# Optimization experiments

Measured on AMD Instinct MI355X. Metric: run time of the kernel, lower is better.

## Reference

```python
import jax, jax.numpy as jnp
import numpy as np

B, T, NH, NB = 16, 400, 100, 65
SR, BLOCK = 16000, 160
REV_LEN = SR  # Reverb(sampling_rate, sampling_rate)


def _fft_convolve(signal, kernel):
    # torch: pad signal right by n, kernel left by its length, multiply spectra, keep 2nd half
    n = signal.shape[-1]
    s = jnp.pad(signal, [(0, 0)] * (signal.ndim - 1) + [(0, n)])
    k = jnp.pad(kernel, [(0, 0)] * (kernel.ndim - 1) + [(kernel.shape[-1], 0)])
    out = jnp.fft.irfft(jnp.fft.rfft(s) * jnp.fft.rfft(k), s.shape[-1])
    return out[..., out.shape[-1] // 2:]


def _amp_to_impulse_response(amp, target_size):
    # amp: [..., n_bands] real magnitudes treated as zero-phase rfft coefficients
    ir = jnp.fft.irfft(jax.lax.complex(amp, jnp.zeros_like(amp)))  # [..., 2*(NB-1)]
    fs = ir.shape[-1]
    ir = jnp.roll(ir, fs // 2, axis=-1)
    win = 0.5 - 0.5 * jnp.cos(2.0 * np.pi * jnp.arange(fs, dtype=ir.dtype) / fs)  # periodic hann
    ir = ir * win
    ir = jnp.pad(ir, [(0, 0)] * (ir.ndim - 1) + [(0, target_size - fs)])
    return jnp.roll(ir, -fs // 2, axis=-1)


def setup_inputs() -> dict:
    key = jax.random.key(0)
    ks = jax.random.split(key, 6)
    pitch = 40.0 + 400.0 * jax.random.uniform(ks[0], (B, T, 1), dtype=jnp.float32)
    total_amp = jax.random.uniform(ks[1], (B, T), dtype=jnp.float32)
    harmo_amps = jax.random.uniform(ks[2], (B, NH, T), dtype=jnp.float32) + 1e-3
    noise_filter = 0.1 * jax.random.uniform(ks[3], (B, T, NB), dtype=jnp.float32)
    noise = 2.0 * jax.random.uniform(ks[4], (B, T, BLOCK), dtype=jnp.float32) - 1.0
    reverb_noise = 2.0 * jax.random.uniform(ks[5], (REV_LEN, 1), dtype=jnp.float32) - 1.0
    decay = jnp.asarray(5.0, jnp.float32)
    wet = jnp.asarray(0.0, jnp.float32)
    return dict(pitch=pitch, total_amp=total_amp, harmo_amps=harmo_amps,
                noise_filter=noise_filter, noise=noise, reverb_noise=reverb_noise,
                decay=decay, wet=wet, sampling_rate=SR, block_size=BLOCK)


def reference(pitch, total_amp, harmo_amps, noise_filter, noise, reverb_noise,
              decay, wet, sampling_rate, block_size):
    dt = pitch.dtype
    n_harm = harmo_amps.shape[1]
    harm_idx = jnp.arange(1, n_harm + 1, dtype=dt)
    # remove_above_nyquist: mask harmonics whose freq >= sr/2 (tiny epsilon kept, as in DDSP)
    freqs = pitch[:, :, 0][:, None, :] * harm_idx[None, :, None]          # [B,NH,T]
    aa = (freqs < (sampling_rate / 2)).astype(dt) + 1e-4
    amps = harmo_amps * aa
    amps = jnp.transpose(amps, (0, 2, 1))                                  # [B,T,NH]
    amps = amps / jnp.sum(amps, axis=-1, keepdims=True)
    amps = amps * total_amp[..., None]
    # nearest-neighbor upsample by block_size (F.interpolate default mode)
    amps_up = jnp.repeat(amps, block_size, axis=1)                         # [B,N,NH]
    pitch_up = jnp.repeat(pitch, block_size, axis=1)                       # [B,N,1]
    # harmonic additive synthesis
    omega = jnp.cumsum(2.0 * np.pi * pitch_up / sampling_rate, axis=1)     # [B,N,1]
    harmonic = jnp.sum(jnp.sin(omega * harm_idx) * amps_up, axis=-1, keepdims=True)
    # filtered noise branch
    impulse = _amp_to_impulse_response(noise_filter, block_size)           # [B,T,BLOCK]
    noise_f = _fft_convolve(noise, impulse)                                # [B,T,BLOCK]
    noise_f = noise_f.reshape(noise_f.shape[0], -1, 1)                     # [B,N,1]
    signal = harmonic + noise_f
    # reverb (forward with reverb=True)
    rev_len = reverb_noise.shape[0]
    t = (jnp.arange(rev_len, dtype=dt) / sampling_rate)[None, :, None]     # [1,L,1]
    imp = reverb_noise[None] * jnp.exp(-jax.nn.softplus(-decay) * t * 500.0) * jax.nn.sigmoid(wet)
    imp = imp.at[:, 0].set(1.0)
    imp = jnp.pad(imp, ((0, 0), (0, signal.shape[1] - rev_len), (0, 0)))   # [1,N,1]
    out = _fft_convolve(signal[..., 0], imp[..., 0])[..., None]            # [B,N,1]
    return out
```

## Files before the change

kernel.cpp:

```cpp
#include <hip/hip_runtime.h>

#define B_ 16
#define T_ 400
#define NH_ 100
#define NB_ 65
#define BLK_ 160
#define SR_ 16000
#define N_ 64000
#define REV_ 16000
#define KPAD_ 16128
#define KTOT_ 80128
#define NT_ 1022
#define KSPLIT_ 8
#define STEPS_ 63
#define M_ 8
#define NWG_ 500

typedef __attribute__((ext_vector_type(8))) _Float16 f16x8;
typedef __attribute__((ext_vector_type(2))) _Float16 f16x2;
typedef __attribute__((ext_vector_type(4))) float f32x4;

#define ROT(c, s, c1, s1)                                   \
  {                                                         \
    float _t = (c) * (s1);                                  \
    float _u = (s) * (s1);                                  \
    float _ns = fmaf((s), (c1), _t);                        \
    (c) = fmaf((c), (c1), -_u);                             \
    (s) = _ns;                                              \
  }

static __device__ __forceinline__ float dot2f(f16x2 a, f16x2 b, float c) {
#if __has_builtin(__builtin_amdgcn_fdot2)
  return __builtin_amdgcn_fdot2(a, b, c, false);
#else
  return fmaf((float)a[0], (float)b[0], fmaf((float)a[1], (float)b[1], c));
#endif
}

__global__ __launch_bounds__(512) void k_pre(const float* __restrict__ pitch,
                                             const float* __restrict__ rn,
                                             const float* __restrict__ dec,
                                             const float* __restrict__ wet,
                                             double* __restrict__ Pv,
                                             double* __restrict__ Xv,
                                             _Float16* __restrict__ FH,
                                             _Float16* __restrict__ PH) {
  const int blk = blockIdx.x, tid = threadIdx.x;
  if (blk >= NT_) {
    __shared__ double s[512];
    const int b = blk - NT_, t = tid;
    double x = 0.0;
    if (t < T_) x = (double)pitch[b * T_ + t] * (1.0 / (double)SR_);
    s[t] = x;
    __syncthreads();
    for (int off = 1; off < 512; off <<= 1) {
      double v = (t >= off) ? s[t - off] : 0.0;
      __syncthreads();
      s[t] += v;
      __syncthreads();
    }
    if (t < T_) {
      Xv[b * T_ + t] = x;
      Pv[b * T_ + t] = (s[t] - x) * 160.0;
    }
    return;
  }
  const int t = blk;
  const int gid = t * 512 + tid;
  if (gid < 32256) ((f32x4*)PH)[gid] = (f32x4){0.f, 0.f, 0.f, 0.f};
  const int lane = tid >> 3, j = tid & 7;
  const int idx = (t - 14) * 16 + (lane & 15) - ((lane >> 4) << 3) - j;
  float v = 0.f;
  if (idx == 0) {
    v = 1.0f;
  } else if (idx > 0 && idx < REV_) {
    const float a = log1pf(expf(-dec[0]));
    const float sg = 1.f / (1.f + expf(-wet[0]));
    v = rn[idx] * expf(-a * ((float)idx / (float)SR_) * 500.0f) * sg;
  }
  FH[t * 512 + tid] = (_Float16)v;
}

__global__ __launch_bounds__(160) void k_synth(
    const float* __restrict__ pitch, const float* __restrict__ tamp,
    const float* __restrict__ harmo, const float* __restrict__ nfilt,
    const float* __restrict__ noise, const double* __restrict__ Pv,
    const double* __restrict__ Xv, _Float16* __restrict__ PH) {
  const int bt = blockIdx.x, b = bt / T_, t = bt - b * T_;
  const int tid = threadIdx.x;
  __shared__ __align__(16) float amp[104];
  __shared__ __align__(16) float a_s[NB_ + 3];
  __shared__ __align__(16) float ir_s[68];
  __shared__ __align__(16) _Float16 C0[320];
  __shared__ __align__(16) _Float16 C1[320];
  __shared__ __align__(16) _Float16 imp_sw[128];
  __shared__ float red_s;

  const float pv = pitch[b * T_ + t];
  int nv = (int)(8000.0f / pv);
  if (nv > NH_) nv = NH_;
  while (nv < NH_ && (float)(nv + 1) * pv < 8000.0f) ++nv;
  while (nv > 0 && (float)nv * pv >= 8000.0f) --nv;

  if (tid < NB_) a_s[tid] = nfilt[bt * NB_ + tid];
  {
    const _Float16 nh = (_Float16)noise[bt * BLK_ + tid];
    C0[160 + tid] = nh;
    C1[159 + tid] = nh;
    C0[tid] = (_Float16)0.f;
    if (tid < 159) C1[tid] = (_Float16)0.f;
  }
  if (tid < NH_) {
    const float ha = harmo[(b * NH_ + tid) * T_ + t];
    const float aa = (pv * (float)(tid + 1) < 8000.0f ? 1.0f : 0.0f) + 1e-4f;
    amp[tid] = ha * aa;
  } else if (tid < 104) {
    amp[tid] = 0.f;
  }
  __syncthreads();

  float irv = 0.f;
  if (tid < 65) {
    const float phi = (float)tid * (1.0f / 128.0f);
    const float c1 = __builtin_amdgcn_cosf(phi);
    const float s1 = __builtin_amdgcn_sinf(phi);
    float c2 = fmaf(c1, c1, -s1 * s1), s2 = 2.f * c1 * s1;
    float c3 = fmaf(c2, c1, -s2 * s1), s3 = fmaf(s2, c1, c2 * s1);
    const float c4 = fmaf(c2, c2, -s2 * s2), s4 = 2.f * c2 * s2;
    float r0c = 1.f, r0s = 0.f;
    float r1c = c1, r1s = s1;
    float r2c = c2, r2s = s2;
    float r3c = c3, r3s = s3;
    float a0 = 0.f, a1 = 0.f, a2 = 0.f, a3 = 0.f;
#pragma unroll
    for (int m = 0; m < 16; ++m) {
      const f32x4 a4 = *(const f32x4*)&a_s[m << 2];
      a0 = fmaf(a4[0], r0c, a0); ROT(r0c, r0s, c4, s4);
      a1 = fmaf(a4[1], r1c, a1); ROT(r1c, r1s, c4, s4);
      a2 = fmaf(a4[2], r2c, a2); ROT(r2c, r2s, c4, s4);
      a3 = fmaf(a4[3], r3c, a3); ROT(r3c, r3s, c4, s4);
    }
    const float accS = (a0 + a1) + (a2 + a3);
    irv = (2.f * accS - a_s[0] + ((tid & 1) ? -a_s[64] : a_s[64])) * (1.0f / 128.0f);
    ir_s[tid] = irv;
  } else if (tid >= 128) {
    const int l = tid - 128;
    float v = amp[l] + amp[l + 32] + amp[l + 64] + (l < 4 ? amp[l + 96] : 0.f);
    v += __shfl_xor(v, 16);
    v += __shfl_xor(v, 8);
    v += __shfl_xor(v, 4);
    v += __shfl_xor(v, 2);
    v += __shfl_xor(v, 1);
    if (l == 0) red_s = v;
  }
  __syncthreads();

  if (tid < 64) {
    const float w = 0.5f + 0.5f * __builtin_amdgcn_cosf((float)tid * (1.0f / 128.0f));
    imp_sw[tid ^ 1] = (_Float16)(w * irv);
  } else if (tid >= 96) {
    const int u = tid - 96;
    const float w = 0.5f - 0.5f * __builtin_amdgcn_cosf((float)u * (1.0f / 128.0f));
    imp_sw[64 + (u ^ 1)] = (_Float16)(w * ir_s[64 - u]);
  }
  const float scale = tamp[b * T_ + t] / red_s;
  double th = Pv[bt] + (double)(tid + 1) * Xv[bt];
  th -= floor(th);
  const float theta = (float)th;
  const float cT = __builtin_amdgcn_cosf(theta);
  const float sT = __builtin_amdgcn_sinf(theta);
  __syncthreads();

  float acc;
  {
    float c2 = fmaf(cT, cT, -sT * sT), s2 = 2.f * cT * sT;
    float c3 = fmaf(c2, cT, -s2 * sT), s3 = fmaf(s2, cT, c2 * sT);
    const float c4 = fmaf(c2, c2, -s2 * s2), s4 = 2.f * c2 * s2;
    float rAc = cT, rAs = sT;
    float rBc = c2, rBs = s2;
    float rCc = c3, rCs = s3;
    float rDc = c4, rDs = s4;
    float a0 = 0.f, a1 = 0.f, a2 = 0.f, a3 = 0.f;
    const int S = (nv + 3) >> 2;
    for (int m = 0; m < S; ++m) {
      const f32x4 a4 = *(const f32x4*)&amp[m << 2];
      a0 = fmaf(a4[0], rAs, a0); ROT(rAc, rAs, c4, s4);
      a1 = fmaf(a4[1], rBs, a1); ROT(rBc, rBs, c4, s4);
      a2 = fmaf(a4[2], rCs, a2); ROT(rCc, rCs, c4, s4);
      a3 = fmaf(a4[3], rDs, a3); ROT(rDc, rDs, c4, s4);
    }
    acc = ((a0 + a1) + (a2 + a3)) * scale;
  }

  float nf = 0.f;
  {
    const f16x2* np0;
    int pe;
    if (tid & 1) {
      np0 = (const f16x2*)C0;
      pe = (159 + tid) >> 1;
    } else {
      np0 = (const f16x2*)C1;
      pe = (158 + tid) >> 1;
    }
    const f16x8* ip = (const f16x8*)imp_sw;
#pragma unroll
    for (int k0 = 0; k0 < 8; ++k0) {
      const f16x8 i8 = ip[k0];
      const int kb = k0 << 2;
      nf = dot2f((f16x2){i8[0], i8[1]}, np0[pe - kb], nf);
      nf = dot2f((f16x2){i8[2], i8[3]}, np0[pe - kb - 1], nf);
      nf = dot2f((f16x2){i8[4], i8[5]}, np0[pe - kb - 2], nf);
      nf = dot2f((f16x2){i8[6], i8[7]}, np0[pe - kb - 3], nf);
    }
#pragma unroll
    for (int k0 = 0; k0 < 8; ++k0) {
      const f16x8 i8 = ip[8 + k0];
      const int kb = (k0 << 2) + 48;
      nf = dot2f((f16x2){i8[0], i8[1]}, np0[pe - kb], nf);
      nf = dot2f((f16x2){i8[2], i8[3]}, np0[pe - kb - 1], nf);
      nf = dot2f((f16x2){i8[4], i8[5]}, np0[pe - kb - 2], nf);
      nf = dot2f((f16x2){i8[6], i8[7]}, np0[pe - kb - 3], nf);
    }
  }

  const float v = acc + nf;
  const unsigned k = (unsigned)(KPAD_ + t * BLK_ + tid);
  const unsigned off = ((k >> 3) << 7) + ((unsigned)b << 3) + (k & 7u);
  PH[off] = (_Float16)v;
}

static __device__ __forceinline__ f32x4 mfma_f16(f16x8 a, f16x8 b, f32x4 c) {
  return __builtin_amdgcn_mfma_f32_16x16x32_f16(a, b, c, 0, 0, 0);
}

template <int U, bool PF>
__device__ __forceinline__ void conv_step(f16x8 (&Rh)[M_], f32x4 (&acc)[M_], f16x8& bhi,
                                          const f16x8* __restrict__ ph,
                                          const f16x8* __restrict__ fh,
                                          int& kcur, int& tcur) {
  f16x8 nbh, na0, na1;
  if (PF) {
    kcur += 64;
    nbh = ph[kcur];
    tcur -= 2;
    na0 = fh[tcur * 64];
    na1 = fh[(tcur + 1) * 64];
  }
#pragma unroll
  for (int m = 0; m < M_; ++m) {
    const int sl = (m - 2 * U) & (M_ - 1);
    acc[m] = mfma_f16(Rh[sl], bhi, acc[m]);
  }
  if (PF) {
    Rh[(M_ - 2 - 2 * U) & (M_ - 1)] = na0;
    Rh[(M_ - 1 - 2 * U) & (M_ - 1)] = na1;
    bhi = nbh;
  }
}

__global__ __launch_bounds__(512) void k_mconv(const f16x8* __restrict__ FH,
                                               const f16x8* __restrict__ PH,
                                               float* __restrict__ out) {
  const int tid = threadIdx.x;
  const int s = tid >> 6, lane = tid & 63;
  int w = blockIdx.x;
  {
    const int q = NWG_ / 8, r = NWG_ % 8;
    const int xcd = w & 7, o = w >> 3;
    w = (xcd < r ? xcd * (q + 1) : r * (q + 1) + (xcd - r) * q) + o;
  }
  const int Q0 = w << 7;
  const int T0 = 1014 - 126 * s;

  const f16x8* fh = FH + lane;
  f16x8 Rh[M_];
#pragma unroll
  for (int m = 0; m < M_; ++m) Rh[m] = fh[(T0 + m) * 64];
  f32x4 acc[M_];
#pragma unroll
  for (int m = 0; m < M_; ++m) acc[m] = (f32x4){0.f, 0.f, 0.f, 0.f};

  const f16x8* ph = PH + ((lane >> 4) << 4) + (lane & 15);
  int kcur = (Q0 + 128 + 2016 * s) << 1;
  int tcur = T0;
  f16x8 bhi = ph[kcur];

  for (int ii = 0; ii < 15; ++ii) {
    conv_step<0, true>(Rh, acc, bhi, ph, fh, kcur, tcur);
    conv_step<1, true>(Rh, acc, bhi, ph, fh, kcur, tcur);
    conv_step<2, true>(Rh, acc, bhi, ph, fh, kcur, tcur);
    conv_step<3, true>(Rh, acc, bhi, ph, fh, kcur, tcur);
  }
  conv_step<0, true>(Rh, acc, bhi, ph, fh, kcur, tcur);
  conv_step<1, true>(Rh, acc, bhi, ph, fh, kcur, tcur);
  conv_step<2, false>(Rh, acc, bhi, ph, fh, kcur, tcur);

  __shared__ f32x4 part[4][M_][64];
  if (s < 4) {
#pragma unroll
    for (int m = 0; m < M_; ++m) part[s][m][lane] = acc[m];
  }
  __syncthreads();
  if (s >= 4) {
#pragma unroll
    for (int m = 0; m < M_; ++m) part[s - 4][m][lane] += acc[m];
  }
  __syncthreads();
  {
    const int m = tid >> 6, ln = tid & 63;
    f32x4 v = part[0][m][ln];
    v += part[1][m][ln];
    v += part[2][m][ln];
    v += part[3][m][ln];
    const int b = ln & 15, g = ln >> 4;
    *(f32x4*)(out + (size_t)b * N_ + Q0 + (m << 4) + (g << 2)) = v;
  }
}

extern "C" void kernel_launch(void* const* d_in, const int* in_sizes, int n_in,
                              void* d_out, int out_size, void* d_ws, size_t ws_size,
                              hipStream_t stream) {
  const float* pitch = (const float*)d_in[0];
  const float* tamp  = (const float*)d_in[1];
  const float* harmo = (const float*)d_in[2];
  const float* nfilt = (const float*)d_in[3];
  const float* noise = (const float*)d_in[4];
  const float* rn    = (const float*)d_in[5];
  const float* dec   = (const float*)d_in[6];
  const float* wet   = (const float*)d_in[7];

  char* ws = (char*)d_ws;
  size_t off = 0;
  _Float16* PH = (_Float16*)(ws + off); off += (size_t)KTOT_ * 16 * 2;
  _Float16* FH = (_Float16*)(ws + off); off += (size_t)NT_ * 512 * 2;
  double* Pv = (double*)(ws + off);     off += (size_t)B_ * T_ * 8;
  double* Xv = (double*)(ws + off);     off += (size_t)B_ * T_ * 8;
  float* out = (float*)d_out;

  k_pre<<<dim3(NT_ + B_), dim3(512), 0, stream>>>(pitch, rn, dec, wet, Pv, Xv, FH, PH);
  k_synth<<<dim3(B_ * T_), dim3(160), 0, stream>>>(pitch, tamp, harmo, nfilt, noise, Pv, Xv, PH);
  k_mconv<<<dim3(NWG_), dim3(512), 0, stream>>>((const f16x8*)FH, (const f16x8*)PH, out);
}
```

Before: 71.10 us.

## Use Chebyshev recurrence for harmonic sums and pack two frames per block

Replaces the complex rotation recurrences (four multiplies per step) in the impulse-response DFT and the harmonic sine sum with a Chebyshev three-term recurrence (one FMA per step), handling eight terms per iteration. The synth kernel now processes two frames per 320-thread workgroup, with shared arrays indexed by group, to halve the block count and improve wave packing. The Chebyshev recurrence may accumulate more rounding error than rotation over the roughly 100 harmonics.

```diff
diff --git a/kernel.cpp b/kernel.cpp
--- a/kernel.cpp
+++ b/kernel.cpp
@@ -19,15 +19,6 @@
 typedef __attribute__((ext_vector_type(8))) _Float16 f16x8;
 typedef __attribute__((ext_vector_type(2))) _Float16 f16x2;
 typedef __attribute__((ext_vector_type(4))) float f32x4;
-
-#define ROT(c, s, c1, s1)                                   \
-  {                                                         \
-    float _t = (c) * (s1);                                  \
-    float _u = (s) * (s1);                                  \
-    float _ns = fmaf((s), (c1), _t);                        \
-    (c) = fmaf((c), (c1), -_u);                             \
-    (s) = _ns;                                              \
-  }
 
 static __device__ __forceinline__ float dot2f(f16x2 a, f16x2 b, float c) {
 #if __has_builtin(__builtin_amdgcn_fdot2)
@@ -81,90 +72,98 @@
   FH[t * 512 + tid] = (_Float16)v;
 }
 
-__global__ __launch_bounds__(160) void k_synth(
+__global__ __launch_bounds__(320) void k_synth(
     const float* __restrict__ pitch, const float* __restrict__ tamp,
     const float* __restrict__ harmo, const float* __restrict__ nfilt,
     const float* __restrict__ noise, const double* __restrict__ Pv,
     const double* __restrict__ Xv, _Float16* __restrict__ PH) {
-  const int bt = blockIdx.x, b = bt / T_, t = bt - b * T_;
   const int tid = threadIdx.x;
-  __shared__ __align__(16) float amp[104];
-  __shared__ __align__(16) float a_s[NB_ + 3];
-  __shared__ __align__(16) float ir_s[68];
-  __shared__ __align__(16) _Float16 C0[320];
-  __shared__ __align__(16) _Float16 C1[320];
-  __shared__ __align__(16) _Float16 imp_sw[128];
-  __shared__ float red_s;
-
-  const float pv = pitch[b * T_ + t];
+  const int g = (tid >= 160) ? 1 : 0;
+  const int ltid = tid - (g << 7) - (g << 5);
+  const int bt = (blockIdx.x << 1) + g;
+  const int b = bt / T_, t = bt - b * T_;
+  __shared__ __align__(16) float amp[2][112];
+  __shared__ __align__(16) float a_s[2][68];
+  __shared__ __align__(16) float ir_s[2][68];
+  __shared__ __align__(16) _Float16 C0[2][320];
+  __shared__ __align__(16) _Float16 C1[2][320];
+  __shared__ __align__(16) _Float16 imp_sw[2][128];
+  __shared__ float red_s[2];
+
+  const float pv = pitch[bt];
   int nv = (int)(8000.0f / pv);
   if (nv > NH_) nv = NH_;
   while (nv < NH_ && (float)(nv + 1) * pv < 8000.0f) ++nv;
   while (nv > 0 && (float)nv * pv >= 8000.0f) --nv;
 
-  if (tid < NB_) a_s[tid] = nfilt[bt * NB_ + tid];
-  {
-    const _Float16 nh = (_Float16)noise[bt * BLK_ + tid];
-    C0[160 + tid] = nh;
-    C1[159 + tid] = nh;
-    C0[tid] = (_Float16)0.f;
-    if (tid < 159) C1[tid] = (_Float16)0.f;
-  }
-  if (tid < NH_) {
-    const float ha = harmo[(b * NH_ + tid) * T_ + t];
-    const float aa = (pv * (float)(tid + 1) < 8000.0f ? 1.0f : 0.0f) + 1e-4f;
-    amp[tid] = ha * aa;
-  } else if (tid < 104) {
-    amp[tid] = 0.f;
+  if (ltid < NB_) a_s[g][ltid] = nfilt[bt * NB_ + ltid];
+  {
+    const _Float16 nh = (_Float16)noise[bt * BLK_ + ltid];
+    C0[g][160 + ltid] = nh;
+    C1[g][159 + ltid] = nh;
+    C0[g][ltid] = (_Float16)0.f;
+    if (ltid < 159) C1[g][ltid] = (_Float16)0.f;
+  }
+  if (ltid < NH_) {
+    const float ha = harmo[(b * NH_ + ltid) * T_ + t];
+    const float aa = (pv * (float)(ltid + 1) < 8000.0f ? 1.0f : 0.0f) + 1e-4f;
+    amp[g][ltid] = ha * aa;
+  } else if (ltid < 112) {
+    amp[g][ltid] = 0.f;
   }
   __syncthreads();
 
   float irv = 0.f;
-  if (tid < 65) {
-    const float phi = (float)tid * (1.0f / 128.0f);
+  if (ltid < 65) {
+    const float phi = (float)ltid * (1.0f / 128.0f);
     const float c1 = __builtin_amdgcn_cosf(phi);
-    const float s1 = __builtin_amdgcn_sinf(phi);
-    float c2 = fmaf(c1, c1, -s1 * s1), s2 = 2.f * c1 * s1;
-    float c3 = fmaf(c2, c1, -s2 * s1), s3 = fmaf(s2, c1, c2 * s1);
-    const float c4 = fmaf(c2, c2, -s2 * s2), s4 = 2.f * c2 * s2;
-    float r0c = 1.f, r0s = 0.f;
-    float r1c = c1, r1s = s1;
-    float r2c = c2, r2s = s2;
-    float r3c = c3, r3s = s3;
+    const float c2 = fmaf(2.f * c1, c1, -1.f);
+    const float c3 = fmaf(2.f * c2, c1, -c1);
+    const float c4 = fmaf(2.f * c2, c2, -1.f);
+    const float tc = 2.f * c4;
+    float x0 = 1.f, p0 = c4;
+    float x1 = c1, p1 = c3;
+    float x2 = c2, p2 = c2;
+    float x3 = c3, p3 = c1;
     float a0 = 0.f, a1 = 0.f, a2 = 0.f, a3 = 0.f;
 #pragma unroll
-    for (int m = 0; m < 16; ++m) {
-      const f32x4 a4 = *(const f32x4*)&a_s[m << 2];
-      a0 = fmaf(a4[0], r0c, a0); ROT(r0c, r0s, c4, s4);
-      a1 = fmaf(a4[1], r1c, a1); ROT(r1c, r1s, c4, s4);
-      a2 = fmaf(a4[2], r2c, a2); ROT(r2c, r2s, c4, s4);
-      a3 = fmaf(a4[3], r3c, a3); ROT(r3c, r3s, c4, s4);
+    for (int m = 0; m < 8; ++m) {
+      const f32x4 aA = *(const f32x4*)&a_s[g][m << 3];
+      const f32x4 aB = *(const f32x4*)&a_s[g][(m << 3) + 4];
+      a0 = fmaf(aA[0], x0, a0); const float y0 = fmaf(tc, x0, -p0);
+      a1 = fmaf(aA[1], x1, a1); const float y1 = fmaf(tc, x1, -p1);
+      a2 = fmaf(aA[2], x2, a2); const float y2 = fmaf(tc, x2, -p2);
+      a3 = fmaf(aA[3], x3, a3); const float y3 = fmaf(tc, x3, -p3);
+      a0 = fmaf(aB[0], y0, a0); const float z0 = fmaf(tc, y0, -x0); p0 = y0; x0 = z0;
+      a1 = fmaf(aB[1], y1, a1); const float z1 = fmaf(tc, y1, -x1); p1 = y1; x1 = z1;
+      a2 = fmaf(aB[2], y2, a2); const float z2 = fmaf(tc, y2, -x2); p2 = y2; x2 = z2;
+      a3 = fmaf(aB[3], y3, a3); const float z3 = fmaf(tc, y3, -x3); p3 = y3; x3 = z3;
     }
     const float accS = (a0 + a1) + (a2 + a3);
-    irv = (2.f * accS - a_s[0] + ((tid & 1) ? -a_s[64] : a_s[64])) * (1.0f / 128.0f);
-    ir_s[tid] = irv;
-  } else if (tid >= 128) {
-    const int l = tid - 128;
-    float v = amp[l] + amp[l + 32] + amp[l + 64] + (l < 4 ? amp[l + 96] : 0.f);
+    irv = (2.f * accS - a_s[g][0] + ((ltid & 1) ? -a_s[g][64] : a_s[g][64])) * (1.0f / 128.0f);
+    ir_s[g][ltid] = irv;
+  } else if (ltid >= 128) {
+    const int l = ltid - 128;
+    float v = amp[g][l] + amp[g][l + 32] + amp[g][l + 64] + (l < 4 ? amp[g][l + 96] : 0.f);
     v += __shfl_xor(v, 16);
     v += __shfl_xor(v, 8);
     v += __shfl_xor(v, 4);
     v += __shfl_xor(v, 2);
     v += __shfl_xor(v, 1);
-    if (l == 0) red_s = v;
-  }
-  __syncthreads();
-
-  if (tid < 64) {
-    const float w = 0.5f + 0.5f * __builtin_amdgcn_cosf((float)tid * (1.0f / 128.0f));
-    imp_sw[tid ^ 1] = (_Float16)(w * irv);
-  } else if (tid >= 96) {
-    const int u = tid - 96;
+    if (l == 0) red_s[g] = v;
+  }
+  __syncthreads();
+
+  if (ltid < 64) {
+    const float w = 0.5f + 0.5f * __builtin_amdgcn_cosf((float)ltid * (1.0f / 128.0f));
+    imp_sw[g][ltid ^ 1] = (_Float16)(w * irv);
+  } else if (ltid >= 96 && ltid < 160) {
+    const int u = ltid - 96;
     const float w = 0.5f - 0.5f * __builtin_amdgcn_cosf((float)u * (1.0f / 128.0f));
-    imp_sw[64 + (u ^ 1)] = (_Float16)(w * ir_s[64 - u]);
-  }
-  const float scale = tamp[b * T_ + t] / red_s;
-  double th = Pv[bt] + (double)(tid + 1) * Xv[bt];
+    imp_sw[g][64 + (u ^ 1)] = (_Float16)(w * ir_s[g][64 - u]);
+  }
+  const float scale = tamp[bt] / red_s[g];
+  double th = Pv[bt] + (double)(ltid + 1) * Xv[bt];
   th -= floor(th);
   const float theta = (float)th;
   const float cT = __builtin_amdgcn_cosf(theta);
@@ -173,21 +172,29 @@
 
   float acc;
   {
-    float c2 = fmaf(cT, cT, -sT * sT), s2 = 2.f * cT * sT;
-    float c3 = fmaf(c2, cT, -s2 * sT), s3 = fmaf(s2, cT, c2 * sT);
-    const float c4 = fmaf(c2, c2, -s2 * s2), s4 = 2.f * c2 * s2;
-    float rAc = cT, rAs = sT;
-    float rBc = c2, rBs = s2;
-    float rCc = c3, rCs = s3;
-    float rDc = c4, rDs = s4;
+    const float c2 = fmaf(cT, cT, -sT * sT);
+    const float s2 = 2.f * cT * sT;
+    const float s3 = fmaf(s2, cT, c2 * sT);
+    const float s4 = 2.f * s2 * c2;
+    const float c4 = fmaf(2.f * c2, c2, -1.f);
+    const float tc = 2.f * c4;
+    float x0 = sT, p0 = -s3;
+    float x1 = s2, p1 = -s2;
+    float x2 = s3, p2 = -sT;
+    float x3 = s4, p3 = 0.f;
     float a0 = 0.f, a1 = 0.f, a2 = 0.f, a3 = 0.f;
-    const int S = (nv + 3) >> 2;
+    const int S = (nv + 7) >> 3;
     for (int m = 0; m < S; ++m) {
-      const f32x4 a4 = *(const f32x4*)&amp[m << 2];
-      a0 = fmaf(a4[0], rAs, a0); ROT(rAc, rAs, c4, s4);
-      a1 = fmaf(a4[1], rBs, a1); ROT(rBc, rBs, c4, s4);
-      a2 = fmaf(a4[2], rCs, a2); ROT(rCc, rCs, c4, s4);
-      a3 = fmaf(a4[3], rDs, a3); ROT(rDc, rDs, c4, s4);
+      const f32x4 aA = *(const f32x4*)&amp[g][m << 3];
+      const f32x4 aB = *(const f32x4*)&amp[g][(m << 3) + 4];
+      a0 = fmaf(aA[0], x0, a0); const float y0 = fmaf(tc, x0, -p0);
+      a1 = fmaf(aA[1], x1, a1); const float y1 = fmaf(tc, x1, -p1);
+      a2 = fmaf(aA[2], x2, a2); const float y2 = fmaf(tc, x2, -p2);
+      a3 = fmaf(aA[3], x3, a3); const float y3 = fmaf(tc, x3, -p3);
+      a0 = fmaf(aB[0], y0, a0); const float z0 = fmaf(tc, y0, -x0); p0 = y0; x0 = z0;
+      a1 = fmaf(aB[1], y1, a1); const float z1 = fmaf(tc, y1, -x1); p1 = y1; x1 = z1;
+      a2 = fmaf(aB[2], y2, a2); const float z2 = fmaf(tc, y2, -x2); p2 = y2; x2 = z2;
+      a3 = fmaf(aB[3], y3, a3); const float z3 = fmaf(tc, y3, -x3); p3 = y3; x3 = z3;
     }
     acc = ((a0 + a1) + (a2 + a3)) * scale;
   }
@@ -196,14 +203,14 @@
   {
     const f16x2* np0;
     int pe;
-    if (tid & 1) {
-      np0 = (const f16x2*)C0;
-      pe = (159 + tid) >> 1;
+    if (ltid & 1) {
+      np0 = (const f16x2*)C0[g];
+      pe = (159 + ltid) >> 1;
     } else {
-      np0 = (const f16x2*)C1;
-      pe = (158 + tid) >> 1;
-    }
-    const f16x8* ip = (const f16x8*)imp_sw;
+      np0 = (const f16x2*)C1[g];
+      pe = (158 + ltid) >> 1;
+    }
+    const f16x8* ip = (const f16x8*)imp_sw[g];
 #pragma unroll
     for (int k0 = 0; k0 < 8; ++k0) {
       const f16x8 i8 = ip[k0];
@@ -225,7 +232,7 @@
   }
 
   const float v = acc + nf;
-  const unsigned k = (unsigned)(KPAD_ + t * BLK_ + tid);
+  const unsigned k = (unsigned)(KPAD_ + t * BLK_ + ltid);
   const unsigned off = ((k >> 3) << 7) + ((unsigned)b << 3) + (k & 7u);
   PH[off] = (_Float16)v;
 }
@@ -339,6 +346,6 @@
   float* out = (float*)d_out;
 
   k_pre<<<dim3(NT_ + B_), dim3(512), 0, stream>>>(pitch, rn, dec, wet, Pv, Xv, FH, PH);
-  k_synth<<<dim3(B_ * T_), dim3(160), 0, stream>>>(pitch, tamp, harmo, nfilt, noise, Pv, Xv, PH);
+  k_synth<<<dim3(B_ * T_ / 2), dim3(320), 0, stream>>>(pitch, tamp, harmo, nfilt, noise, Pv, Xv, PH);
   k_mconv<<<dim3(NWG_), dim3(512), 0, stream>>>((const f16x8*)FH, (const f16x8*)PH, out);
 }
```

After: 68.27 us. 4.0% less time.
